# Kernel optimization log

Measured on AMD Instinct MI355X. Metric: run time of the kernel, lower is better.

Reference implementation:

```python
import jax, jax.numpy as jnp
import numpy as np

IN_F, OUT_F, TASK_D, RANK, HID = 1024, 1024, 256, 8, 64
ALPHA = 8.0
SCALING = ALPHA / RANK  # 1.0


def setup_inputs() -> dict:
    key = jax.random.key(0)
    ks = jax.random.split(key, 12)
    s = 0.02
    return {
        "x": jax.random.normal(ks[0], (4, 2048, IN_F), dtype=jnp.float32),
        "base_out": jax.random.normal(ks[1], (4, 2048, OUT_F), dtype=jnp.float32),
        "task_emb": jax.random.normal(ks[2], (4, TASK_D), dtype=jnp.float32),
        # gen_a MLP: Linear(task_dim->hid) + GELU + Linear(hid->out*r)
        "Wa1": jax.random.normal(ks[3], (HID, TASK_D), dtype=jnp.float32) * s,
        "ba1": jnp.zeros((HID,), dtype=jnp.float32),
        "Wa2": jax.random.normal(ks[4], (OUT_F * RANK, HID), dtype=jnp.float32) * s,
        "ba2": jnp.zeros((OUT_F * RANK,), dtype=jnp.float32),
        # gen_b MLP: Linear(task_dim->hid) + GELU + Linear(hid->r*in)
        "Wb1": jax.random.normal(ks[5], (HID, TASK_D), dtype=jnp.float32) * s,
        "bb1": jnp.zeros((HID,), dtype=jnp.float32),
        "Wb2": jax.random.normal(ks[6], (RANK * IN_F, HID), dtype=jnp.float32) * s,
        "bb2": jnp.zeros((RANK * IN_F,), dtype=jnp.float32),
    }


def reference(x, base_out, task_emb, Wa1, ba1, Wa2, ba2, Wb1, bb1, Wb2, bb2):
    lead = x.shape[:-1]
    x2d = x.reshape(-1, IN_F)                      # (b_eff, in)
    b_eff = x2d.shape[0]
    # broadcast task_emb to b_eff rows (repeat + trim, as in torch)
    B = task_emb.shape[0]
    reps = (b_eff + B - 1) // B
    task_eff = jnp.tile(task_emb, (reps, 1))[:b_eff]  # (b_eff, task_dim)

    gelu = lambda t: jax.nn.gelu(t, approximate=False)
    h_a = gelu(task_eff @ Wa1.T + ba1)
    vec_a = h_a @ Wa2.T + ba2                      # (b_eff, out*r)
    h_b = gelu(task_eff @ Wb1.T + bb1)
    vec_b = h_b @ Wb2.T + bb2                      # (b_eff, r*in)

    a = vec_a.reshape(b_eff, OUT_F, RANK)
    b = vec_b.reshape(b_eff, RANK, IN_F)

    # dropout p=0 (eval): x passes through
    tmp = jnp.einsum('bi,bri->br', x2d, b)         # (b_eff, r)
    y_delta = jnp.einsum('br,bor->bo', tmp, a)     # (b_eff, out)
    y = base_out.reshape(-1, OUT_F) + SCALING * y_delta
    return y.reshape(*lead, OUT_F)
```

## Files before the change

### kernel.cpp

```cpp
#include <hip/hip_runtime.h>
#include <math.h>

#define IN_F   1024
#define OUT_F  1024
#define TASK_D 256
#define RANK   8
#define HID    64

__device__ __forceinline__ float gelu_exact(float v) {
    return 0.5f * v * (1.0f + erff(v * 0.70710678118654752f));
}

__global__ __launch_bounds__(256) void gen_kernel(
    const float* __restrict__ task_emb,
    const float* __restrict__ Wa1, const float* __restrict__ ba1,
    const float* __restrict__ Wa2, const float* __restrict__ ba2,
    const float* __restrict__ Wb1, const float* __restrict__ bb1,
    const float* __restrict__ Wb2, const float* __restrict__ bb2,
    float* __restrict__ vec_a_t, float* __restrict__ vec_b)
{
    const int gen = blockIdx.x >> 7;
    const int blk = blockIdx.x & 127;
    const float* __restrict__ W1 = gen ? Wb1 : Wa1;
    const float* __restrict__ b1 = gen ? bb1 : ba1;
    const float* __restrict__ W2 = gen ? Wb2 : Wa2;
    const float* __restrict__ b2 = gen ? bb2 : ba2;

    __shared__ float hs[4][HID];
    {
        const int j = threadIdx.x >> 2;
        const int t = threadIdx.x & 3;
        const float4* te = (const float4*)(task_emb + t * TASK_D);
        const float4* w  = (const float4*)(W1 + j * TASK_D);
        float acc = 0.f;
        #pragma unroll
        for (int d = 0; d < TASK_D / 4; ++d) {
            float4 a = te[d], b = w[d];
            acc += a.x * b.x + a.y * b.y + a.z * b.z + a.w * b.w;
        }
        hs[t][j] = gelu_exact(acc + b1[j]);
    }
    __syncthreads();

    const int lrow = threadIdx.x >> 2;
    const int q    = threadIdx.x & 3;
    const int o    = blk * 64 + lrow;

    const float4* w2 = (const float4*)(W2 + (size_t)o * HID + q * 16);
    float acc0 = 0.f, acc1 = 0.f, acc2 = 0.f, acc3 = 0.f;
    #pragma unroll
    for (int k = 0; k < 4; ++k) {
        float4 w = w2[k];
        const int kb = q * 16 + k * 4;
        acc0 += hs[0][kb] * w.x + hs[0][kb+1] * w.y + hs[0][kb+2] * w.z + hs[0][kb+3] * w.w;
        acc1 += hs[1][kb] * w.x + hs[1][kb+1] * w.y + hs[1][kb+2] * w.z + hs[1][kb+3] * w.w;
        acc2 += hs[2][kb] * w.x + hs[2][kb+1] * w.y + hs[2][kb+2] * w.z + hs[2][kb+3] * w.w;
        acc3 += hs[3][kb] * w.x + hs[3][kb+1] * w.y + hs[3][kb+2] * w.z + hs[3][kb+3] * w.w;
    }
    #pragma unroll
    for (int off = 1; off <= 2; off <<= 1) {
        acc0 += __shfl_xor(acc0, off, 64);
        acc1 += __shfl_xor(acc1, off, 64);
        acc2 += __shfl_xor(acc2, off, 64);
        acc3 += __shfl_xor(acc3, off, 64);
    }
    if (q == 0) {
        const float bb = b2[o];
        float v[4] = { acc0 + bb, acc1 + bb, acc2 + bb, acc3 + bb };
        if (gen == 0) {
            const int oo = o >> 3, r = o & 7;
            #pragma unroll
            for (int t = 0; t < 4; ++t)
                vec_a_t[t * (RANK * OUT_F) + r * OUT_F + oo] = v[t];
        } else {
            #pragma unroll
            for (int t = 0; t < 4; ++t)
                vec_b[t * (RANK * IN_F) + o] = v[t];
        }
    }
}

__global__ __launch_bounds__(256) void apply_kernel(
    const float* __restrict__ x, const float* __restrict__ base_out,
    const float* __restrict__ vec_a_t, const float* __restrict__ vec_b,
    float* __restrict__ out)
{
    const int t    = blockIdx.x & 3;
    const int g    = blockIdx.x >> 2;
    const int wave = threadIdx.x >> 6;
    const int lane = threadIdx.x & 63;

    __shared__ float bs[RANK * IN_F];
    {
        const float4* src = (const float4*)(vec_b + (size_t)t * (RANK * IN_F));
        float4* dst = (float4*)bs;
        #pragma unroll
        for (int i = 0; i < 8; ++i)
            dst[threadIdx.x + 256 * i] = src[threadIdx.x + 256 * i];
    }

    const int jbase = g * 8 + wave * 2;
    const int row0  = t + 4 * jbase;
    const int row1  = row0 + 4;

    float4 xv[2][4];
    {
        const float* __restrict__ xr0 = x + (size_t)row0 * IN_F;
        const float* __restrict__ xr1 = x + (size_t)row1 * IN_F;
        #pragma unroll
        for (int c = 0; c < 4; ++c) {
            xv[0][c] = *(const float4*)(xr0 + c * 256 + lane * 4);
            xv[1][c] = *(const float4*)(xr1 + c * 256 + lane * 4);
        }
    }

    __syncthreads();

    float acc[2][RANK];
    #pragma unroll
    for (int i = 0; i < 2; ++i)
        #pragma unroll
        for (int r = 0; r < RANK; ++r) acc[i][r] = 0.f;

    #pragma unroll
    for (int c = 0; c < 4; ++c) {
        const int k = c * 256 + lane * 4;
        #pragma unroll
        for (int r = 0; r < RANK; ++r) {
            const float4 bv = *(const float4*)(bs + r * IN_F + k);
            acc[0][r] += xv[0][c].x * bv.x + xv[0][c].y * bv.y
                       + xv[0][c].z * bv.z + xv[0][c].w * bv.w;
            acc[1][r] += xv[1][c].x * bv.x + xv[1][c].y * bv.y
                       + xv[1][c].z * bv.z + xv[1][c].w * bv.w;
        }
    }

    #pragma unroll
    for (int off = 32; off > 0; off >>= 1) {
        #pragma unroll
        for (int i = 0; i < 2; ++i)
            #pragma unroll
            for (int r = 0; r < RANK; ++r)
                acc[i][r] += __shfl_xor(acc[i][r], off, 64);
    }

    const float* __restrict__ at = vec_a_t + (size_t)t * (RANK * OUT_F);
    const float* __restrict__ br0 = base_out + (size_t)row0 * OUT_F;
    const float* __restrict__ br1 = base_out + (size_t)row1 * OUT_F;
    float*       __restrict__ or0 = out + (size_t)row0 * OUT_F;
    float*       __restrict__ or1 = out + (size_t)row1 * OUT_F;

    float4 bo[2][4];
    #pragma unroll
    for (int c = 0; c < 4; ++c) {
        const int o = c * 256 + lane * 4;
        bo[0][c] = *(const float4*)(br0 + o);
        bo[1][c] = *(const float4*)(br1 + o);
    }

    #pragma unroll
    for (int c = 0; c < 4; ++c) {
        const int o = c * 256 + lane * 4;
        float4 rv0 = bo[0][c];
        float4 rv1 = bo[1][c];
        #pragma unroll
        for (int r = 0; r < RANK; ++r) {
            const float4 af = *(const float4*)(at + r * OUT_F + o);
            rv0.x += acc[0][r] * af.x;  rv0.y += acc[0][r] * af.y;
            rv0.z += acc[0][r] * af.z;  rv0.w += acc[0][r] * af.w;
            rv1.x += acc[1][r] * af.x;  rv1.y += acc[1][r] * af.y;
            rv1.z += acc[1][r] * af.z;  rv1.w += acc[1][r] * af.w;
        }
        *(float4*)(or0 + o) = rv0;
        *(float4*)(or1 + o) = rv1;
    }
}

extern "C" void kernel_launch(void* const* d_in, const int* in_sizes, int n_in,
                              void* d_out, int out_size, void* d_ws, size_t ws_size,
                              hipStream_t stream) {
    const float* x        = (const float*)d_in[0];
    const float* base_out = (const float*)d_in[1];
    const float* task_emb = (const float*)d_in[2];
    const float* Wa1      = (const float*)d_in[3];
    const float* ba1      = (const float*)d_in[4];
    const float* Wa2      = (const float*)d_in[5];
    const float* ba2      = (const float*)d_in[6];
    const float* Wb1      = (const float*)d_in[7];
    const float* bb1      = (const float*)d_in[8];
    const float* Wb2      = (const float*)d_in[9];
    const float* bb2      = (const float*)d_in[10];
    float* out = (float*)d_out;

    float* vec_a_t = (float*)d_ws;
    float* vec_b   = vec_a_t + 4 * RANK * OUT_F;

    const int b_eff = in_sizes[0] / IN_F;

    gen_kernel<<<256, 256, 0, stream>>>(task_emb, Wa1, ba1, Wa2, ba2,
                                        Wb1, bb1, Wb2, bb2, vec_a_t, vec_b);
    apply_kernel<<<b_eff / 8, 256, 0, stream>>>(x, base_out, vec_a_t, vec_b, out);
}
```

Baseline: 144.8 us.

## Split apply kernel into rank-projection and epilogue kernels with nontemporal accesses

Splits the fused apply kernel in two. The first kernel computes the rank-8 projection of x and writes it to a small workspace buffer. The second kernel keeps the task's A factor in registers and streams base_out to out, using nontemporal loads and stores for the large streaming arrays. This is meant to cut register pressure and the repeated per-row reloads of vec_a from the epilogue, and to avoid cache pollution. The cost is an extra kernel launch plus a workspace round trip for tmp, and x and base_out are no longer streamed concurrently in one kernel.

```diff
diff --git a/kernel.cpp b/kernel.cpp
--- a/kernel.cpp
+++ b/kernel.cpp
@@ -6,6 +6,8 @@
 #define TASK_D 256
 #define RANK   8
 #define HID    64
+
+typedef float vfloat4 __attribute__((ext_vector_type(4)));
 
 __device__ __forceinline__ float gelu_exact(float v) {
     return 0.5f * v * (1.0f + erff(v * 0.70710678118654752f));
@@ -80,10 +82,9 @@
     }
 }
 
-__global__ __launch_bounds__(256) void apply_kernel(
-    const float* __restrict__ x, const float* __restrict__ base_out,
-    const float* __restrict__ vec_a_t, const float* __restrict__ vec_b,
-    float* __restrict__ out)
+__global__ __launch_bounds__(256) void tmp_kernel(
+    const float* __restrict__ x, const float* __restrict__ vec_b,
+    float* __restrict__ tmp)
 {
     const int t    = blockIdx.x & 3;
     const int g    = blockIdx.x >> 2;
@@ -99,18 +100,18 @@
             dst[threadIdx.x + 256 * i] = src[threadIdx.x + 256 * i];
     }
 
-    const int jbase = g * 8 + wave * 2;
-    const int row0  = t + 4 * jbase;
-    const int row1  = row0 + 4;
-
-    float4 xv[2][4];
+    const int j    = g * 8 + wave * 2;
+    const int row0 = t + 4 * j;
+    const int row1 = row0 + 4;
+
+    vfloat4 xv[2][4];
     {
         const float* __restrict__ xr0 = x + (size_t)row0 * IN_F;
         const float* __restrict__ xr1 = x + (size_t)row1 * IN_F;
         #pragma unroll
         for (int c = 0; c < 4; ++c) {
-            xv[0][c] = *(const float4*)(xr0 + c * 256 + lane * 4);
-            xv[1][c] = *(const float4*)(xr1 + c * 256 + lane * 4);
+            xv[0][c] = __builtin_nontemporal_load((const vfloat4*)(xr0 + c * 256 + lane * 4));
+            xv[1][c] = __builtin_nontemporal_load((const vfloat4*)(xr1 + c * 256 + lane * 4));
         }
     }
 
@@ -144,35 +145,66 @@
                 acc[i][r] += __shfl_xor(acc[i][r], off, 64);
     }
 
-    const float* __restrict__ at = vec_a_t + (size_t)t * (RANK * OUT_F);
-    const float* __restrict__ br0 = base_out + (size_t)row0 * OUT_F;
-    const float* __restrict__ br1 = base_out + (size_t)row1 * OUT_F;
-    float*       __restrict__ or0 = out + (size_t)row0 * OUT_F;
-    float*       __restrict__ or1 = out + (size_t)row1 * OUT_F;
-
-    float4 bo[2][4];
-    #pragma unroll
-    for (int c = 0; c < 4; ++c) {
-        const int o = c * 256 + lane * 4;
-        bo[0][c] = *(const float4*)(br0 + o);
-        bo[1][c] = *(const float4*)(br1 + o);
-    }
-
-    #pragma unroll
-    for (int c = 0; c < 4; ++c) {
-        const int o = c * 256 + lane * 4;
-        float4 rv0 = bo[0][c];
-        float4 rv1 = bo[1][c];
-        #pragma unroll
-        for (int r = 0; r < RANK; ++r) {
-            const float4 af = *(const float4*)(at + r * OUT_F + o);
-            rv0.x += acc[0][r] * af.x;  rv0.y += acc[0][r] * af.y;
-            rv0.z += acc[0][r] * af.z;  rv0.w += acc[0][r] * af.w;
-            rv1.x += acc[1][r] * af.x;  rv1.y += acc[1][r] * af.y;
-            rv1.z += acc[1][r] * af.z;  rv1.w += acc[1][r] * af.w;
-        }
-        *(float4*)(or0 + o) = rv0;
-        *(float4*)(or1 + o) = rv1;
+    #pragma unroll
+    for (int i = 0; i < 2; ++i) {
+        float v = acc[i][0];
+        #pragma unroll
+        for (int r = 1; r < RANK; ++r)
+            if (lane == r) v = acc[i][r];
+        if (lane < RANK) {
+            const int row = (i == 0) ? row0 : row1;
+            tmp[(size_t)row * RANK + lane] = v;
+        }
+    }
+}
+
+__global__ __launch_bounds__(256) void ep_kernel(
+    const float* __restrict__ base_out, const float* __restrict__ tmp,
+    const float* __restrict__ vec_a_t, float* __restrict__ out)
+{
+    const int t    = blockIdx.x & 3;
+    const int u    = blockIdx.x >> 2;
+    const int wave = threadIdx.x >> 6;
+    const int lane = threadIdx.x & 63;
+    const int o    = wave * 256 + lane * 4;
+
+    const float* __restrict__ at = vec_a_t + (size_t)t * (RANK * OUT_F) + o;
+    float4 af[RANK];
+    #pragma unroll
+    for (int r = 0; r < RANK; ++r)
+        af[r] = *(const float4*)(at + r * OUT_F);
+
+    #pragma unroll
+    for (int half = 0; half < 2; ++half) {
+        int rows[4];
+        #pragma unroll
+        for (int i = 0; i < 4; ++i)
+            rows[i] = t + 4 * (u * 8 + half * 4 + i);
+
+        float4 tp0[4], tp1[4];
+        vfloat4 bo[4];
+        #pragma unroll
+        for (int i = 0; i < 4; ++i) {
+            const float4* tpp = (const float4*)(tmp + (size_t)rows[i] * RANK);
+            tp0[i] = tpp[0];
+            tp1[i] = tpp[1];
+            bo[i]  = __builtin_nontemporal_load(
+                        (const vfloat4*)(base_out + (size_t)rows[i] * OUT_F + o));
+        }
+
+        #pragma unroll
+        for (int i = 0; i < 4; ++i) {
+            vfloat4 rv = bo[i];
+            rv.x += tp0[i].x * af[0].x + tp0[i].y * af[1].x + tp0[i].z * af[2].x + tp0[i].w * af[3].x
+                  + tp1[i].x * af[4].x + tp1[i].y * af[5].x + tp1[i].z * af[6].x + tp1[i].w * af[7].x;
+            rv.y += tp0[i].x * af[0].y + tp0[i].y * af[1].y + tp0[i].z * af[2].y + tp0[i].w * af[3].y
+                  + tp1[i].x * af[4].y + tp1[i].y * af[5].y + tp1[i].z * af[6].y + tp1[i].w * af[7].y;
+            rv.z += tp0[i].x * af[0].z + tp0[i].y * af[1].z + tp0[i].z * af[2].z + tp0[i].w * af[3].z
+                  + tp1[i].x * af[4].z + tp1[i].y * af[5].z + tp1[i].z * af[6].z + tp1[i].w * af[7].z;
+            rv.w += tp0[i].x * af[0].w + tp0[i].y * af[1].w + tp0[i].z * af[2].w + tp0[i].w * af[3].w
+                  + tp1[i].x * af[4].w + tp1[i].y * af[5].w + tp1[i].z * af[6].w + tp1[i].w * af[7].w;
+            __builtin_nontemporal_store(rv, (vfloat4*)(out + (size_t)rows[i] * OUT_F + o));
+        }
     }
 }
 
@@ -194,10 +226,12 @@
 
     float* vec_a_t = (float*)d_ws;
     float* vec_b   = vec_a_t + 4 * RANK * OUT_F;
+    float* tmp     = vec_b   + 4 * RANK * IN_F;
 
     const int b_eff = in_sizes[0] / IN_F;
 
     gen_kernel<<<256, 256, 0, stream>>>(task_emb, Wa1, ba1, Wa2, ba2,
                                         Wb1, bb1, Wb2, bb2, vec_a_t, vec_b);
-    apply_kernel<<<b_eff / 8, 256, 0, stream>>>(x, base_out, vec_a_t, vec_b, out);
-}
+    tmp_kernel<<<b_eff / 8, 256, 0, stream>>>(x, vec_b, tmp);
+    ep_kernel<<<b_eff / 8, 256, 0, stream>>>(base_out, tmp, vec_a_t, out);
+}
```

Result: no change. 146.6 us (+1.2%).
